# Performance work log

Measured on AMD Instinct MI355X. Metric: run time of the kernel, lower is better.

The kernel has to match this reference:

```python
import jax, jax.numpy as jnp
import numpy as np

B, C, H, W = 8, 256, 32, 32
L, G, K = 4, 4, 2048
D = C // G


def setup_inputs() -> dict:
    key = jax.random.key(0)
    k1, k2 = jax.random.split(key)
    x = jax.random.normal(k1, (B, C, H, W), dtype=jnp.float32)
    # per-level, per-group codebooks: [L, G, K, D]
    codebooks = jax.random.normal(k2, (L, G, K, D), dtype=jnp.float32)
    return {"x": x, "codebooks": codebooks}


def _quantize(r, cb):
    """One quantization stage.
    r : [B, G, N, D] residual features (N = H*W)
    cb: [G, K, D]    per-group codebook
    Returns straight-through quantized codes q: [B, G, N, D].
    """
    # squared euclidean distance ||r - c||^2, expanded form (avoids [.,.,D] broadcast blowup)
    d2 = (jnp.sum(r * r, axis=-1, keepdims=True)
          - 2.0 * jnp.einsum('bgnd,gkd->bgnk', r, cb)
          + jnp.sum(cb * cb, axis=-1)[None, :, None, :])  # [B,G,N,K]
    logits = -d2
    probs = jax.nn.softmax(logits, axis=-1)
    idx = jnp.argmax(probs, axis=-1)                       # argmin distance
    hard = jax.nn.one_hot(idx, cb.shape[1], dtype=r.dtype)
    # OneHotCategoricalStraightThrough (mode): hard fwd, soft grad
    ste = hard + probs - jax.lax.stop_gradient(probs)
    return jnp.einsum('bgnk,gkd->bgnd', ste, cb)


def reference(x, codebooks):
    b, c, h, w = x.shape
    l, g, k, d = codebooks.shape
    # split channels into groups: [B, G, D, H*W] -> [B, G, N, D]
    r = x.reshape(b, g, d, h * w).transpose(0, 1, 3, 2)
    xhat = jnp.zeros_like(r)
    for i in range(l):  # small fixed number of cascade levels
        q = _quantize(r, codebooks[i])
        xhat = xhat + q
        r = r - q  # residual passed to next level
    return xhat.transpose(0, 1, 3, 2).reshape(b, c, h, w)
```

## Files before the change

### kernel.cpp

```cpp
#include <hip/hip_runtime.h>

#define NB 8
#define NC 256
#define NHW 1024
#define NL 4
#define NG 4
#define NK 2048
#define ND 64

#define RS 68
#define CS 72

typedef __attribute__((ext_vector_type(8))) _Float16 f16x8;
typedef __attribute__((ext_vector_type(4))) _Float16 f16x4;
typedef __attribute__((ext_vector_type(4))) float    f32x4;

__device__ __forceinline__ void fsplit(float v, _Float16& h, _Float16& l) {
    _Float16 hh = (_Float16)v;
    h = hh;
    l = (_Float16)(v - (float)hh);
}

__global__ void cq_prep_kernel(const float* __restrict__ cb,
                               _Float16* __restrict__ wfrag,
                               float* __restrict__ cn) {
    int wv   = (blockIdx.x * 256 + threadIdx.x) >> 6;
    int lane = threadIdx.x & 63;
    int l4 = lane & 15, l16 = lane >> 4;
    int lg = wv >> 7, kt = wv & 127;
    int k  = kt * 16 + l4;
    const float* src = cb + ((size_t)lg * NK + k) * ND;

    float4 a0 = *(const float4*)(src + l16 * 8);
    float4 a1 = *(const float4*)(src + l16 * 8 + 4);
    float4 b0 = *(const float4*)(src + 32 + l16 * 8);
    float4 b1 = *(const float4*)(src + 32 + l16 * 8 + 4);

    f16x8 h0, lo0, h1, lo1;
    _Float16 h, lo;
    fsplit(a0.x,h,lo); h0[0]=h; lo0[0]=lo;  fsplit(a0.y,h,lo); h0[1]=h; lo0[1]=lo;
    fsplit(a0.z,h,lo); h0[2]=h; lo0[2]=lo;  fsplit(a0.w,h,lo); h0[3]=h; lo0[3]=lo;
    fsplit(a1.x,h,lo); h0[4]=h; lo0[4]=lo;  fsplit(a1.y,h,lo); h0[5]=h; lo0[5]=lo;
    fsplit(a1.z,h,lo); h0[6]=h; lo0[6]=lo;  fsplit(a1.w,h,lo); h0[7]=h; lo0[7]=lo;
    fsplit(b0.x,h,lo); h1[0]=h; lo1[0]=lo;  fsplit(b0.y,h,lo); h1[1]=h; lo1[1]=lo;
    fsplit(b0.z,h,lo); h1[2]=h; lo1[2]=lo;  fsplit(b0.w,h,lo); h1[3]=h; lo1[3]=lo;
    fsplit(b1.x,h,lo); h1[4]=h; lo1[4]=lo;  fsplit(b1.y,h,lo); h1[5]=h; lo1[5]=lo;
    fsplit(b1.z,h,lo); h1[6]=h; lo1[6]=lo;  fsplit(b1.w,h,lo); h1[7]=h; lo1[7]=lo;

    _Float16* outp = wfrag + (size_t)wv * 2048;
    *(f16x8*)(outp +    0 + lane * 8) = h0;
    *(f16x8*)(outp +  512 + lane * 8) = h1;
    *(f16x8*)(outp + 1024 + lane * 8) = lo0;
    *(f16x8*)(outp + 1536 + lane * 8) = lo1;

    float s = a0.x*a0.x + a0.y*a0.y + a0.z*a0.z + a0.w*a0.w
            + a1.x*a1.x + a1.y*a1.y + a1.z*a1.z + a1.w*a1.w
            + b0.x*b0.x + b0.y*b0.y + b0.z*b0.z + b0.w*b0.w
            + b1.x*b1.x + b1.y*b1.y + b1.z*b1.z + b1.w*b1.w;
    s += __shfl_xor(s, 16, 64);
    s += __shfl_xor(s, 32, 64);
    if (l16 == 0) cn[(size_t)lg * NK + k] = 0.5f * s;
}

__global__ __launch_bounds__(256, 2) void cq_main7_kernel(
    const float* __restrict__ x, const float* __restrict__ cb,
    const _Float16* __restrict__ wfrag, const float* __restrict__ cn,
    float* __restrict__ out)
{
    __shared__ float r_lds[32][RS];
    __shared__ float mv_lds[4][32];
    __shared__ int   mi_lds[4][32];
    __shared__ int   ks_lds[32];

    const int tid = threadIdx.x;
    const int blk = (blockIdx.x & 7) * 128 + (blockIdx.x >> 3);
    const int nt  = blk & 31;
    const int g   = (blk >> 5) & 3;
    const int b   = blk >> 7;
    const int n0  = nt * 32;

    const float* xb = x + ((size_t)(b * NC + g * ND)) * NHW + n0;
#pragma unroll
    for (int dd = 0; dd < 2; ++dd) {
        int d = (tid >> 3) + dd * 32;
        int n = (tid & 7) * 4;
        float4 xv = *(const float4*)(&xb[(size_t)d * NHW + n]);
        r_lds[n + 0][d] = xv.x; r_lds[n + 1][d] = xv.y;
        r_lds[n + 2][d] = xv.z; r_lds[n + 3][d] = xv.w;
    }
    __syncthreads();

    const int lane = tid & 63;
    const int kq   = tid >> 6;
    const int l4   = lane & 15;
    const int l16  = lane >> 4;
    const int kbase = kq * 512;

    for (int l = 0; l < NL; ++l) {
        const float* cbl_g = cb + (size_t)(l * NG + g) * NK * ND;
        const float* cnl   = cn + (size_t)(l * NG + g) * NK;
        const _Float16* fb = wfrag + ((size_t)(l * NG + g) * 128 + kq * 32) * 2048;

        f16x8 ah[2][2], al[2][2];
#pragma unroll
        for (int ns = 0; ns < 2; ++ns) {
#pragma unroll
            for (int c = 0; c < 2; ++c) {
                const float* rp = &r_lds[ns * 16 + l4][c * 32 + l16 * 8];
                float4 v0 = *(const float4*)(rp);
                float4 v1 = *(const float4*)(rp + 4);
                _Float16 h, lo; f16x8 hv, lv;
                fsplit(-v0.x,h,lo); hv[0]=h; lv[0]=lo;
                fsplit(-v0.y,h,lo); hv[1]=h; lv[1]=lo;
                fsplit(-v0.z,h,lo); hv[2]=h; lv[2]=lo;
                fsplit(-v0.w,h,lo); hv[3]=h; lv[3]=lo;
                fsplit(-v1.x,h,lo); hv[4]=h; lv[4]=lo;
                fsplit(-v1.y,h,lo); hv[5]=h; lv[5]=lo;
                fsplit(-v1.z,h,lo); hv[6]=h; lv[6]=lo;
                fsplit(-v1.w,h,lo); hv[7]=h; lv[7]=lo;
                ah[ns][c] = hv; al[ns][c] = lv;
            }
        }

        float minv[2][4];
        int   mini[2][4];
#pragma unroll
        for (int i = 0; i < 2; ++i)
#pragma unroll
            for (int j = 0; j < 4; ++j) { minv[i][j] = 3.4e38f; mini[i][j] = 0; }

        f16x8 c0, c1, c2, c3; float cv;
        {
            const _Float16* p = fb + lane * 8;
            c0 = *(const f16x8*)(p);
            c1 = *(const f16x8*)(p + 512);
            c2 = *(const f16x8*)(p + 1024);
            c3 = *(const f16x8*)(p + 1536);
            cv = cnl[kbase + l4];
        }

#pragma unroll 2
        for (int s = 0; s < 32; ++s) {
            f16x8 p0 = c0, p1 = c1, p2 = c2, p3 = c3; float pv = cv;
            if (s < 31) {
                const _Float16* p = fb + (size_t)(s + 1) * 2048 + lane * 8;
                c0 = *(const f16x8*)(p);
                c1 = *(const f16x8*)(p + 512);
                c2 = *(const f16x8*)(p + 1024);
                c3 = *(const f16x8*)(p + 1536);
                cv = cnl[kbase + (s + 1) * 16 + l4];
            }
            const int kabs = kbase + s * 16 + l4;
            f32x4 acc[2];
#pragma unroll
            for (int ns = 0; ns < 2; ++ns) acc[ns] = (f32x4){pv, pv, pv, pv};
#pragma unroll
            for (int ns = 0; ns < 2; ++ns) {
                acc[ns] = __builtin_amdgcn_mfma_f32_16x16x32_f16(ah[ns][0], p0, acc[ns], 0, 0, 0);
                acc[ns] = __builtin_amdgcn_mfma_f32_16x16x32_f16(ah[ns][1], p1, acc[ns], 0, 0, 0);
                acc[ns] = __builtin_amdgcn_mfma_f32_16x16x32_f16(ah[ns][0], p2, acc[ns], 0, 0, 0);
                acc[ns] = __builtin_amdgcn_mfma_f32_16x16x32_f16(ah[ns][1], p3, acc[ns], 0, 0, 0);
                acc[ns] = __builtin_amdgcn_mfma_f32_16x16x32_f16(al[ns][0], p0, acc[ns], 0, 0, 0);
                acc[ns] = __builtin_amdgcn_mfma_f32_16x16x32_f16(al[ns][1], p1, acc[ns], 0, 0, 0);
            }
#pragma unroll
            for (int ns = 0; ns < 2; ++ns)
#pragma unroll
                for (int j = 0; j < 4; ++j) {
                    float sc = acc[ns][j];
                    bool lt = sc < minv[ns][j];
                    minv[ns][j] = lt ? sc : minv[ns][j];
                    mini[ns][j] = lt ? kabs : mini[ns][j];
                }
        }

#pragma unroll
        for (int m = 1; m < 16; m <<= 1) {
#pragma unroll
            for (int ns = 0; ns < 2; ++ns)
#pragma unroll
                for (int j = 0; j < 4; ++j) {
                    float ov = __shfl_xor(minv[ns][j], m, 64);
                    int   oi = __shfl_xor(mini[ns][j], m, 64);
                    if (ov < minv[ns][j] || (ov == minv[ns][j] && oi < mini[ns][j])) {
                        minv[ns][j] = ov; mini[ns][j] = oi;
                    }
                }
        }
        if (l4 == 0) {
#pragma unroll
            for (int ns = 0; ns < 2; ++ns)
#pragma unroll
                for (int j = 0; j < 4; ++j) {
                    int row = ns * 16 + l16 * 4 + j;
                    mv_lds[kq][row] = minv[ns][j];
                    mi_lds[kq][row] = mini[ns][j];
                }
        }
        __syncthreads();
        if (tid < 32) {
            float bv = mv_lds[0][tid]; int bi = mi_lds[0][tid];
#pragma unroll
            for (int q = 1; q < 4; ++q) {
                float v = mv_lds[q][tid];
                if (v < bv) { bv = v; bi = mi_lds[q][tid]; }
            }
            ks_lds[tid] = bi;
        }
        __syncthreads();

        {
            int row = tid >> 3, dc = (tid & 7) * 8;
            int kw = ks_lds[row];
            const float* qp = cbl_g + (size_t)kw * ND + dc;
#pragma unroll
            for (int i = 0; i < 2; ++i) {
                float4 q  = *(const float4*)(qp + i * 4);
                float* rp = &r_lds[row][dc + i * 4];
                float4 rv = *(float4*)rp;
                rv.x -= q.x; rv.y -= q.y; rv.z -= q.z; rv.w -= q.w;
                *(float4*)rp = rv;
            }
        }
        __syncthreads();
    }

    float* ob = out + ((size_t)(b * NC + g * ND)) * NHW + n0;
#pragma unroll
    for (int dd = 0; dd < 2; ++dd) {
        int d = (tid >> 3) + dd * 32;
        int n = (tid & 7) * 4;
        float4 xv = *(const float4*)(&xb[(size_t)d * NHW + n]);
        float4 ov;
        ov.x = xv.x - r_lds[n + 0][d];
        ov.y = xv.y - r_lds[n + 1][d];
        ov.z = xv.z - r_lds[n + 2][d];
        ov.w = xv.w - r_lds[n + 3][d];
        *(float4*)(&ob[(size_t)d * NHW + n]) = ov;
    }
}

__global__ void cq_cnorm_kernel(const float* __restrict__ cb, float* __restrict__ cn) {
    int idx = blockIdx.x * 256 + threadIdx.x;
    const float4* p = reinterpret_cast<const float4*>(cb + (size_t)idx * ND);
    float s = 0.f;
#pragma unroll
    for (int i = 0; i < ND / 4; ++i) {
        float4 v = p[i];
        s += v.x * v.x + v.y * v.y + v.z * v.z + v.w * v.w;
    }
    cn[idx] = 0.5f * s;
}

__global__ __launch_bounds__(256, 1) void cq_main_kernel(
    const float* __restrict__ x, const float* __restrict__ cb,
    const float* __restrict__ cn, float* __restrict__ out)
{
    __shared__ float    r_lds[128][RS];
    __shared__ _Float16 cbh_lds[2][128][CS];
    __shared__ _Float16 cbl_lds[2][128][CS];
    __shared__ float    mv_lds[2][128];
    __shared__ int      mi_lds[2][128];
    __shared__ int      ks_lds[128];

    const int tid = threadIdx.x;
    const int blk = blockIdx.x;
    const int nt  = blk & 7;
    const int bg  = blk >> 3;
    const int g   = bg & 3;
    const int b   = bg >> 2;
    const int n0  = nt * 128;

    const float* xb = x + ((size_t)(b * NC + g * ND)) * NHW + n0;
#pragma unroll
    for (int dd = 0; dd < 8; ++dd) {
        int d = (tid >> 5) + dd * 8;
        int n = (tid & 31) * 4;
        float4 xv = *reinterpret_cast<const float4*>(&xb[(size_t)d * NHW + n]);
        r_lds[n + 0][d] = xv.x; r_lds[n + 1][d] = xv.y;
        r_lds[n + 2][d] = xv.z; r_lds[n + 3][d] = xv.w;
    }

    const int lane = tid & 63;
    const int wid  = tid >> 6;
    const int rg   = wid & 1;
    const int kh   = wid >> 1;
    const int l4   = lane & 15;
    const int l16  = lane >> 4;

    __syncthreads();

    for (int l = 0; l < NL; ++l) {
        const float* cbl_g = cb + (size_t)(l * NG + g) * NK * ND;
        const float* cnl   = cn + (size_t)(l * NG + g) * NK;

        f16x8 ah[4][2], al[4][2];
#pragma unroll
        for (int ns = 0; ns < 4; ++ns) {
#pragma unroll
            for (int c = 0; c < 2; ++c) {
                const float* rp = &r_lds[rg * 64 + ns * 16 + l4][c * 32 + l16 * 8];
                float4 v0 = *reinterpret_cast<const float4*>(rp);
                float4 v1 = *reinterpret_cast<const float4*>(rp + 4);
                _Float16 h, lo; f16x8 hv, lv;
                fsplit(-v0.x, h, lo); hv[0] = h; lv[0] = lo;
                fsplit(-v0.y, h, lo); hv[1] = h; lv[1] = lo;
                fsplit(-v0.z, h, lo); hv[2] = h; lv[2] = lo;
                fsplit(-v0.w, h, lo); hv[3] = h; lv[3] = lo;
                fsplit(-v1.x, h, lo); hv[4] = h; lv[4] = lo;
                fsplit(-v1.y, h, lo); hv[5] = h; lv[5] = lo;
                fsplit(-v1.z, h, lo); hv[6] = h; lv[6] = lo;
                fsplit(-v1.w, h, lo); hv[7] = h; lv[7] = lo;
                ah[ns][c] = hv; al[ns][c] = lv;
            }
        }

        float minv[4][4];
        int   mini[4][4];
#pragma unroll
        for (int i = 0; i < 4; ++i)
#pragma unroll
            for (int j = 0; j < 4; ++j) { minv[i][j] = 3.4e38f; mini[i][j] = 0; }

        float4 sreg[8];
#pragma unroll
        for (int p = 0; p < 8; ++p) {
            int kk = p * 16 + (tid >> 4);
            int kg = (kk < 64) ? kk : (1024 - 64 + kk);
            sreg[p] = *reinterpret_cast<const float4*>(&cbl_g[(size_t)kg * ND + (tid & 15) * 4]);
        }
#pragma unroll
        for (int p = 0; p < 8; ++p) {
            int kk = p * 16 + (tid >> 4);
            float4 v = sreg[p];
            _Float16 h, lo; f16x4 hv, lv;
            fsplit(v.x, h, lo); hv[0] = h; lv[0] = lo;
            fsplit(v.y, h, lo); hv[1] = h; lv[1] = lo;
            fsplit(v.z, h, lo); hv[2] = h; lv[2] = lo;
            fsplit(v.w, h, lo); hv[3] = h; lv[3] = lo;
            *reinterpret_cast<f16x4*>(&cbh_lds[0][kk][(tid & 15) * 4]) = hv;
            *reinterpret_cast<f16x4*>(&cbl_lds[0][kk][(tid & 15) * 4]) = lv;
        }

        for (int s = 0; s < 16; ++s) {
            __syncthreads();

            if (s < 15) {
#pragma unroll
                for (int p = 0; p < 8; ++p) {
                    int kk = p * 16 + (tid >> 4);
                    int kg = (kk < 64) ? ((s + 1) * 64 + kk) : (1024 + (s + 1) * 64 + (kk - 64));
                    sreg[p] = *reinterpret_cast<const float4*>(&cbl_g[(size_t)kg * ND + (tid & 15) * 4]);
                }
            }

            const int buf = s & 1;
            for (int ks = 0; ks < 4; ++ks) {
                int lrow = kh * 64 + ks * 16 + l4;
                int kabs = kh * 1024 + s * 64 + ks * 16 + l4;
                f16x8 bh0 = *reinterpret_cast<const f16x8*>(&cbh_lds[buf][lrow][l16 * 8]);
                f16x8 bh1 = *reinterpret_cast<const f16x8*>(&cbh_lds[buf][lrow][32 + l16 * 8]);
                f16x8 bl0 = *reinterpret_cast<const f16x8*>(&cbl_lds[buf][lrow][l16 * 8]);
                f16x8 bl1 = *reinterpret_cast<const f16x8*>(&cbl_lds[buf][lrow][32 + l16 * 8]);
                float cnv = cnl[kabs];
                f32x4 acc[4];
#pragma unroll
                for (int ns = 0; ns < 4; ++ns) acc[ns] = (f32x4){cnv, cnv, cnv, cnv};
#pragma unroll
                for (int ns = 0; ns < 4; ++ns) {
                    acc[ns] = __builtin_amdgcn_mfma_f32_16x16x32_f16(ah[ns][0], bh0, acc[ns], 0, 0, 0);
                    acc[ns] = __builtin_amdgcn_mfma_f32_16x16x32_f16(ah[ns][1], bh1, acc[ns], 0, 0, 0);
                    acc[ns] = __builtin_amdgcn_mfma_f32_16x16x32_f16(ah[ns][0], bl0, acc[ns], 0, 0, 0);
                    acc[ns] = __builtin_amdgcn_mfma_f32_16x16x32_f16(ah[ns][1], bl1, acc[ns], 0, 0, 0);
                    acc[ns] = __builtin_amdgcn_mfma_f32_16x16x32_f16(al[ns][0], bh0, acc[ns], 0, 0, 0);
                    acc[ns] = __builtin_amdgcn_mfma_f32_16x16x32_f16(al[ns][1], bh1, acc[ns], 0, 0, 0);
                }
#pragma unroll
                for (int ns = 0; ns < 4; ++ns)
#pragma unroll
                    for (int j = 0; j < 4; ++j) {
                        float sc = acc[ns][j];
                        bool lt = sc < minv[ns][j];
                        minv[ns][j] = lt ? sc : minv[ns][j];
                        mini[ns][j] = lt ? kabs : mini[ns][j];
                    }
            }

            if (s < 15) {
                const int nbuf = (s + 1) & 1;
#pragma unroll
                for (int p = 0; p < 8; ++p) {
                    int kk = p * 16 + (tid >> 4);
                    float4 v = sreg[p];
                    _Float16 h, lo; f16x4 hv, lv;
                    fsplit(v.x, h, lo); hv[0] = h; lv[0] = lo;
                    fsplit(v.y, h, lo); hv[1] = h; lv[1] = lo;
                    fsplit(v.z, h, lo); hv[2] = h; lv[2] = lo;
                    fsplit(v.w, h, lo); hv[3] = h; lv[3] = lo;
                    *reinterpret_cast<f16x4*>(&cbh_lds[nbuf][kk][(tid & 15) * 4]) = hv;
                    *reinterpret_cast<f16x4*>(&cbl_lds[nbuf][kk][(tid & 15) * 4]) = lv;
                }
            }
        }

#pragma unroll
        for (int m = 1; m < 16; m <<= 1) {
#pragma unroll
            for (int ns = 0; ns < 4; ++ns)
#pragma unroll
                for (int j = 0; j < 4; ++j) {
                    float ov = __shfl_xor(minv[ns][j], m, 64);
                    int   oi = __shfl_xor(mini[ns][j], m, 64);
                    if (ov < minv[ns][j] || (ov == minv[ns][j] && oi < mini[ns][j])) {
                        minv[ns][j] = ov; mini[ns][j] = oi;
                    }
                }
        }
        if (l4 == 0) {
#pragma unroll
            for (int ns = 0; ns < 4; ++ns)
#pragma unroll
                for (int j = 0; j < 4; ++j) {
                    int row = rg * 64 + ns * 16 + l16 * 4 + j;
                    mv_lds[kh][row] = minv[ns][j];
                    mi_lds[kh][row] = mini[ns][j];
                }
        }
        __syncthreads();
        if (tid < 128) {
            float v0 = mv_lds[0][tid], v1 = mv_lds[1][tid];
            ks_lds[tid] = (v1 < v0) ? mi_lds[1][tid] : mi_lds[0][tid];
        }
        __syncthreads();

        {
            int n  = tid >> 1;
            int db = (tid & 1) * 32;
            int kw = ks_lds[n];
            const float* qp = &cbl_g[(size_t)kw * ND + db];
#pragma unroll
            for (int i = 0; i < 8; ++i) {
                float4 q  = *reinterpret_cast<const float4*>(&qp[i * 4]);
                float* rp = &r_lds[n][db + i * 4];
                float4 rv = *reinterpret_cast<float4*>(rp);
                rv.x -= q.x; rv.y -= q.y; rv.z -= q.z; rv.w -= q.w;
                *reinterpret_cast<float4*>(rp) = rv;
            }
        }
        __syncthreads();
    }

    float* ob = out + ((size_t)(b * NC + g * ND)) * NHW + n0;
#pragma unroll
    for (int dd = 0; dd < 8; ++dd) {
        int d = (tid >> 5) + dd * 8;
        int n = (tid & 31) * 4;
        float4 xv = *reinterpret_cast<const float4*>(&xb[(size_t)d * NHW + n]);
        float4 ov;
        ov.x = xv.x - r_lds[n + 0][d];
        ov.y = xv.y - r_lds[n + 1][d];
        ov.z = xv.z - r_lds[n + 2][d];
        ov.w = xv.w - r_lds[n + 3][d];
        *reinterpret_cast<float4*>(&ob[(size_t)d * NHW + n]) = ov;
    }
}

extern "C" void kernel_launch(void* const* d_in, const int* in_sizes, int n_in,
                              void* d_out, int out_size, void* d_ws, size_t ws_size,
                              hipStream_t stream) {
    const float* x  = (const float*)d_in[0];
    const float* cb = (const float*)d_in[1];
    float* out = (float*)d_out;

    const size_t FRAG_BYTES = (size_t)NL * NG * NK * ND * 2 * 2;
    const size_t NEED = FRAG_BYTES + (size_t)NL * NG * NK * 4;

    if (ws_size >= NEED) {
        _Float16* wfrag = (_Float16*)d_ws;
        float* cn = (float*)((char*)d_ws + FRAG_BYTES);
        cq_prep_kernel<<<512, 256, 0, stream>>>(cb, wfrag, cn);
        cq_main7_kernel<<<NB * NG * (NHW / 32), 256, 0, stream>>>(x, cb, wfrag, cn, out);
    } else {
        float* cn = (float*)d_ws;
        cq_cnorm_kernel<<<(NL * NG * NK) / 256, 256, 0, stream>>>(cb, cn);
        cq_main_kernel<<<NB * NG * (NHW / 128), 256, 0, stream>>>(x, cb, cn, out);
    }
}
```

Baseline: 122.2 us.

## Ping-pong double-buffer codebook fragment loads with sched barriers and higher occupancy

Replaces the single-register prefetch loop with an explicit X/Y ping-pong: each half-iteration issues the next tile's fragment loads, then runs the 12 MFMAs on the other buffer, with sched_barrier fences so the compiler keeps loads ahead of math. MFMA blocks are wrapped in s_setprio raises so compute waves get issue priority. Launch bounds move from 2 to 4 blocks per CU, which caps register use and may cause spilling given the doubled fragment buffers. The aim is better hiding of global load latency behind matrix work.

```diff
diff --git a/kernel.cpp b/kernel.cpp
--- a/kernel.cpp
+++ b/kernel.cpp
@@ -62,7 +62,7 @@
     if (l16 == 0) cn[(size_t)lg * NK + k] = 0.5f * s;
 }
 
-__global__ __launch_bounds__(256, 2) void cq_main7_kernel(
+__global__ __launch_bounds__(256, 4) void cq_main9_kernel(
     const float* __restrict__ x, const float* __restrict__ cb,
     const _Float16* __restrict__ wfrag, const float* __restrict__ cn,
     float* __restrict__ out)
@@ -99,7 +99,6 @@
     for (int l = 0; l < NL; ++l) {
         const float* cbl_g = cb + (size_t)(l * NG + g) * NK * ND;
         const float* cnl   = cn + (size_t)(l * NG + g) * NK;
-        const _Float16* fb = wfrag + ((size_t)(l * NG + g) * 128 + kq * 32) * 2048;
 
         f16x8 ah[2][2], al[2][2];
 #pragma unroll
@@ -129,49 +128,61 @@
 #pragma unroll
             for (int j = 0; j < 4; ++j) { minv[i][j] = 3.4e38f; mini[i][j] = 0; }
 
-        f16x8 c0, c1, c2, c3; float cv;
-        {
-            const _Float16* p = fb + lane * 8;
-            c0 = *(const f16x8*)(p);
-            c1 = *(const f16x8*)(p + 512);
-            c2 = *(const f16x8*)(p + 1024);
-            c3 = *(const f16x8*)(p + 1536);
-            cv = cnl[kbase + l4];
-        }
-
+        const _Float16* ph = wfrag + ((size_t)(l * NG + g) * 128 + kq * 32) * 2048
+                           + lane * 8;
+        const float*    pc = cnl + kbase + l4;
+        int kcur = kbase + l4;
+
+        f16x8 Xh[2], Xl[2], Yh[2], Yl[2];
+        float cvX, cvY;
+
+        auto LD = [&](f16x8 (&H)[2], f16x8 (&L)[2], float& cv) {
+            H[0] = *(const f16x8*)(ph);
+            H[1] = *(const f16x8*)(ph + 512);
+            L[0] = *(const f16x8*)(ph + 1024);
+            L[1] = *(const f16x8*)(ph + 1536);
+            cv = *pc;
+            ph += 2048; pc += 16;
+        };
+
+        auto ST = [&](const f16x8 (&H)[2], const f16x8 (&L)[2], float cv) {
+            f32x4 a0 = {cv, cv, cv, cv};
+            f32x4 a1 = {cv, cv, cv, cv};
+            __builtin_amdgcn_s_setprio(1);
+            a0 = __builtin_amdgcn_mfma_f32_16x16x32_f16(ah[0][0], H[0], a0, 0, 0, 0);
+            a0 = __builtin_amdgcn_mfma_f32_16x16x32_f16(ah[0][1], H[1], a0, 0, 0, 0);
+            a0 = __builtin_amdgcn_mfma_f32_16x16x32_f16(ah[0][0], L[0], a0, 0, 0, 0);
+            a0 = __builtin_amdgcn_mfma_f32_16x16x32_f16(ah[0][1], L[1], a0, 0, 0, 0);
+            a0 = __builtin_amdgcn_mfma_f32_16x16x32_f16(al[0][0], H[0], a0, 0, 0, 0);
+            a0 = __builtin_amdgcn_mfma_f32_16x16x32_f16(al[0][1], H[1], a0, 0, 0, 0);
+            a1 = __builtin_amdgcn_mfma_f32_16x16x32_f16(ah[1][0], H[0], a1, 0, 0, 0);
+            a1 = __builtin_amdgcn_mfma_f32_16x16x32_f16(ah[1][1], H[1], a1, 0, 0, 0);
+            a1 = __builtin_amdgcn_mfma_f32_16x16x32_f16(ah[1][0], L[0], a1, 0, 0, 0);
+            a1 = __builtin_amdgcn_mfma_f32_16x16x32_f16(ah[1][1], L[1], a1, 0, 0, 0);
+            a1 = __builtin_amdgcn_mfma_f32_16x16x32_f16(al[1][0], H[0], a1, 0, 0, 0);
+            a1 = __builtin_amdgcn_mfma_f32_16x16x32_f16(al[1][1], H[1], a1, 0, 0, 0);
+            __builtin_amdgcn_s_setprio(0);
+#pragma unroll
+            for (int j = 0; j < 4; ++j) {
+                bool lt0 = a0[j] < minv[0][j];
+                minv[0][j] = lt0 ? a0[j] : minv[0][j];
+                mini[0][j] = lt0 ? kcur : mini[0][j];
+                bool lt1 = a1[j] < minv[1][j];
+                minv[1][j] = lt1 ? a1[j] : minv[1][j];
+                mini[1][j] = lt1 ? kcur : mini[1][j];
+            }
+            kcur += 16;
+        };
+
+        LD(Xh, Xl, cvX);
 #pragma unroll 2
-        for (int s = 0; s < 32; ++s) {
-            f16x8 p0 = c0, p1 = c1, p2 = c2, p3 = c3; float pv = cv;
-            if (s < 31) {
-                const _Float16* p = fb + (size_t)(s + 1) * 2048 + lane * 8;
-                c0 = *(const f16x8*)(p);
-                c1 = *(const f16x8*)(p + 512);
-                c2 = *(const f16x8*)(p + 1024);
-                c3 = *(const f16x8*)(p + 1536);
-                cv = cnl[kbase + (s + 1) * 16 + l4];
-            }
-            const int kabs = kbase + s * 16 + l4;
-            f32x4 acc[2];
-#pragma unroll
-            for (int ns = 0; ns < 2; ++ns) acc[ns] = (f32x4){pv, pv, pv, pv};
-#pragma unroll
-            for (int ns = 0; ns < 2; ++ns) {
-                acc[ns] = __builtin_amdgcn_mfma_f32_16x16x32_f16(ah[ns][0], p0, acc[ns], 0, 0, 0);
-                acc[ns] = __builtin_amdgcn_mfma_f32_16x16x32_f16(ah[ns][1], p1, acc[ns], 0, 0, 0);
-                acc[ns] = __builtin_amdgcn_mfma_f32_16x16x32_f16(ah[ns][0], p2, acc[ns], 0, 0, 0);
-                acc[ns] = __builtin_amdgcn_mfma_f32_16x16x32_f16(ah[ns][1], p3, acc[ns], 0, 0, 0);
-                acc[ns] = __builtin_amdgcn_mfma_f32_16x16x32_f16(al[ns][0], p0, acc[ns], 0, 0, 0);
-                acc[ns] = __builtin_amdgcn_mfma_f32_16x16x32_f16(al[ns][1], p1, acc[ns], 0, 0, 0);
-            }
-#pragma unroll
-            for (int ns = 0; ns < 2; ++ns)
-#pragma unroll
-                for (int j = 0; j < 4; ++j) {
-                    float sc = acc[ns][j];
-                    bool lt = sc < minv[ns][j];
-                    minv[ns][j] = lt ? sc : minv[ns][j];
-                    mini[ns][j] = lt ? kabs : mini[ns][j];
-                }
+        for (int i = 0; i < 16; ++i) {
+            LD(Yh, Yl, cvY);
+            __builtin_amdgcn_sched_barrier(0);
+            ST(Xh, Xl, cvX);
+            if (i < 15) LD(Xh, Xl, cvX);
+            __builtin_amdgcn_sched_barrier(0);
+            ST(Yh, Yl, cvY);
         }
 
 #pragma unroll
@@ -479,7 +490,7 @@
         _Float16* wfrag = (_Float16*)d_ws;
         float* cn = (float*)((char*)d_ws + FRAG_BYTES);
         cq_prep_kernel<<<512, 256, 0, stream>>>(cb, wfrag, cn);
-        cq_main7_kernel<<<NB * NG * (NHW / 32), 256, 0, stream>>>(x, cb, wfrag, cn, out);
+        cq_main9_kernel<<<NB * NG * (NHW / 32), 256, 0, stream>>>(x, cb, wfrag, cn, out);
     } else {
         float* cn = (float*)d_ws;
         cq_cnorm_kernel<<<(NL * NG * NK) / 256, 256, 0, stream>>>(cb, cn);
```

New measurement: 124.8 us. 2.1% more time.
